# Kernel optimization log

Hardware: AMD Instinct MI355X
Metric: run time of the kernel (lower is better)

## Reference

```python
import jax, jax.numpy as jnp
import numpy as np

N, D, H, E, K = 65536, 128, 256, 32, 2


def setup_inputs() -> dict:
    key = jax.random.key(0)
    ks = jax.random.split(key, 7)
    s_in = 1.0 / np.sqrt(D)
    s_hid = 1.0 / np.sqrt(H)
    return {
        "x": jax.random.normal(ks[0], (N, D), dtype=jnp.float32),
        "W1": jax.random.uniform(ks[1], (E, D, H), jnp.float32, -s_in, s_in),
        "b1": jax.random.uniform(ks[2], (E, H), jnp.float32, -s_in, s_in),
        "W2": jax.random.uniform(ks[3], (E, H, D), jnp.float32, -s_hid, s_hid),
        "b2": jax.random.uniform(ks[4], (E, D), jnp.float32, -s_hid, s_hid),
        "Wr": jax.random.uniform(ks[5], (D, E), jnp.float32, -s_in, s_in),
        "br": jax.random.uniform(ks[6], (E,), jnp.float32, -s_in, s_in),
    }


def reference(x, W1, b1, W2, b2, Wr, br):
    # Router (eval mode: no gate noise)
    logits = x @ Wr + br                                  # [N, E]
    scores = jax.nn.softmax(logits, axis=-1)              # [N, E]
    topk_vals, topk_inds = jax.lax.top_k(scores, K)       # [N, K]

    # dispatch_mask: zeros scattered with top-k probs (scatter_ on dim 1)
    n = x.shape[0]
    dispatch_mask = jnp.zeros_like(scores).at[
        jnp.arange(n)[:, None], topk_inds
    ].set(topk_vals)                                      # [N, E]

    # Dense all-experts compute, as in the reference torch.stack
    h = jax.nn.relu(jnp.einsum("nd,edh->neh", x, W1) + b1)   # [N, E, H]
    expert_outputs = jnp.einsum("neh,ehd->ned", h, W2) + b2  # [N, E, D]

    output = jnp.einsum("ned,ne->nd", expert_outputs, dispatch_mask)  # [N, D]

    importance = dispatch_mask.sum(axis=0)                # [E]
    imp_mean = jnp.mean(importance)
    imp_var = jnp.var(importance, ddof=1)                 # torch.var is unbiased
    load_balancing_loss = imp_var / (imp_mean ** 2 + 1e-9)
    return output, load_balancing_loss
```

## Files before the change

### kernel.cpp

```cpp
#include <hip/hip_runtime.h>
#include <hip/hip_bf16.h>
#include <cstdint>
#include <cstddef>

#define N_TOK 65536
#define DIM 128
#define HID 256
#define NE 32
#define TOPK 2

typedef __bf16 bf16x8 __attribute__((ext_vector_type(8)));
typedef float f32x4 __attribute__((ext_vector_type(4)));
typedef unsigned uint4v __attribute__((ext_vector_type(4)));

__device__ __forceinline__ unsigned short f2bf(float f) {
  unsigned u = __builtin_bit_cast(unsigned, f);
  u += 0x7fffu + ((u >> 16) & 1u);
  return (unsigned short)(u >> 16);
}
__device__ __forceinline__ float bf2f(unsigned s) {
  return __builtin_bit_cast(float, s << 16);
}
__device__ __forceinline__ uint2 split2(float f0, float f1) {
  unsigned u0 = __builtin_bit_cast(unsigned, f0);
  unsigned u1 = __builtin_bit_cast(unsigned, f1);
  unsigned hi = (u0 >> 16) | (u1 & 0xffff0000u);
  float r0 = f0 - __builtin_bit_cast(float, u0 & 0xffff0000u);
  float r1 = f1 - __builtin_bit_cast(float, u1 & 0xffff0000u);
  unsigned lo = (__builtin_bit_cast(unsigned, r0) >> 16) |
                (__builtin_bit_cast(unsigned, r1) & 0xffff0000u);
  uint2 ret; ret.x = hi; ret.y = lo;
  return ret;
}

__global__ void k_zero_out(float* __restrict__ out) {
  int t = blockIdx.x * 256 + threadIdx.x;
  float4 z = make_float4(0.f, 0.f, 0.f, 0.f);
  float4* o4 = (float4*)out;
  o4[t] = z;
  o4[t + 1048576] = z;
}

__global__ void k_weights(const float* __restrict__ W1, const float* __restrict__ W2,
                          const float* __restrict__ Wr,
                          unsigned short* __restrict__ w1t, unsigned short* __restrict__ w2t,
                          double* __restrict__ wrt64, unsigned short* __restrict__ wrb,
                          float* __restrict__ ws32, int* __restrict__ n_suspect) {
  int b = blockIdx.x;
  if (b == 512) {
    if (threadIdx.x == 0) *n_suspect = 0;
#pragma unroll
    for (int j = 0; j < 16; ++j) {
      int idx = j * 256 + threadIdx.x;
      int e = idx >> 7, d = idx & 127;
      wrt64[idx] = (double)Wr[d * NE + e];
    }
#pragma unroll
    for (int j = 0; j < 16; ++j) {
      int idx = j * 256 + threadIdx.x;
      int k = idx >> 5, e = idx & 31;
      float w = Wr[k * NE + e];
      unsigned u = __builtin_bit_cast(unsigned, w);
      unsigned short hs = (unsigned short)(u >> 16);
      float r = w - __builtin_bit_cast(float, u & 0xffff0000u);
      unsigned short ls = (unsigned short)(__builtin_bit_cast(unsigned, r) >> 16);
      int nt = e >> 4, n = e & 15, kc = k >> 5, q = (k >> 3) & 3, jj = k & 7;
      size_t base = ((((size_t)nt * 4 + kc) * 4 + q) * 16 + n) * 8 + jj;
      wrb[base] = hs;
      wrb[8192 + base] = ls;
    }
    return;
  }
  if (b == 0 && threadIdx.x < 96) ws32[threadIdx.x] = 0.f;
  const float* in;
  unsigned short* out;
  int K, r0, c0;
  if (b < 256) {
    int e = b >> 3, tt = b & 7;
    in = W1 + (size_t)e * DIM * HID;
    out = w1t + (size_t)e * DIM * HID;
    K = HID;
    r0 = (tt >> 2) * 64; c0 = (tt & 3) * 64;
  } else {
    b -= 256;
    int e = b >> 3, tt = b & 7;
    in = W2 + (size_t)e * HID * DIM;
    out = w2t + (size_t)e * HID * DIM;
    K = DIM;
    r0 = (tt >> 1) * 64; c0 = (tt & 1) * 64;
  }
  __shared__ float tile[64][65];
  int t2 = threadIdx.x;
  int r = t2 >> 2, cs = (t2 & 3) * 16;
  const float* src = in + (size_t)(r0 + r) * K + c0 + cs;
#pragma unroll
  for (int j = 0; j < 4; ++j) {
    float4 v = *(const float4*)(src + j * 4);
    tile[r][cs + j * 4 + 0] = v.x;
    tile[r][cs + j * 4 + 1] = v.y;
    tile[r][cs + j * 4 + 2] = v.z;
    tile[r][cs + j * 4 + 3] = v.w;
  }
  __syncthreads();
#pragma unroll
  for (int p = 0; p < 2; ++p) {
    int orow = p * 32 + (t2 >> 3);
    int oc8 = (t2 & 7) * 8;
    int rr = r0 + oc8;
    unsigned pk[4];
#pragma unroll
    for (int q = 0; q < 4; ++q) {
      unsigned lo = f2bf(tile[oc8 + 2 * q][orow]);
      unsigned hi = f2bf(tile[oc8 + 2 * q + 1][orow]);
      pk[q] = lo | (hi << 16);
    }
    uint4 u;
    u.x = pk[0]; u.y = pk[1]; u.z = pk[2]; u.w = pk[3];
    size_t addr = (size_t)(rr >> 5) * (K * 32) + (size_t)(c0 + orow) * 32 + (rr & 31);
    *(uint4*)(out + addr) = u;
  }
}

__global__ __launch_bounds__(256) void k_router(
    const float* __restrict__ x, const unsigned short* __restrict__ wrb,
    const float* __restrict__ br, int* __restrict__ top_idx, float* __restrict__ top_val,
    int* __restrict__ suspects, int* __restrict__ n_suspect) {
  int t = threadIdx.x;
  int w = t >> 6, l = t & 63, quad = l >> 4, l15 = l & 15;
  int tok0 = blockIdx.x * 256 + w * 64;

  bf16x8 bfr[2][2][4];
#pragma unroll
  for (int s = 0; s < 2; ++s)
#pragma unroll
    for (int nt = 0; nt < 2; ++nt)
#pragma unroll
      for (int kc = 0; kc < 4; ++kc)
        bfr[s][nt][kc] = *(const bf16x8*)(wrb + s * 8192 +
                          ((((size_t)nt * 4 + kc) * 4 + quad) * 16 + l15) * 8);

  f32x4 acc[4][2];
#pragma unroll
  for (int a = 0; a < 4; ++a)
#pragma unroll
    for (int b = 0; b < 2; ++b) {
      f32x4 z = {0.f, 0.f, 0.f, 0.f};
      acc[a][b] = z;
    }

#pragma unroll
  for (int mt = 0; mt < 4; ++mt) {
    const float* xp = x + (size_t)(tok0 + mt * 16 + l15) * DIM + quad * 8;
    float4 va[4][2];
#pragma unroll
    for (int kc = 0; kc < 4; ++kc) {
      const float4* p = (const float4*)(xp + kc * 32);
      va[kc][0] = p[0];
      va[kc][1] = p[1];
    }
#pragma unroll
    for (int kc = 0; kc < 4; ++kc) {
      uint2 s0 = split2(va[kc][0].x, va[kc][0].y);
      uint2 s1 = split2(va[kc][0].z, va[kc][0].w);
      uint2 s2 = split2(va[kc][1].x, va[kc][1].y);
      uint2 s3 = split2(va[kc][1].z, va[kc][1].w);
      uint4v hu, lu;
      hu[0] = s0.x; lu[0] = s0.y;
      hu[1] = s1.x; lu[1] = s1.y;
      hu[2] = s2.x; lu[2] = s2.y;
      hu[3] = s3.x; lu[3] = s3.y;
      bf16x8 ahi = __builtin_bit_cast(bf16x8, hu);
      bf16x8 alo = __builtin_bit_cast(bf16x8, lu);
#pragma unroll
      for (int nt = 0; nt < 2; ++nt) {
        acc[mt][nt] = __builtin_amdgcn_mfma_f32_16x16x32_bf16(ahi, bfr[0][nt][kc], acc[mt][nt], 0, 0, 0);
        acc[mt][nt] = __builtin_amdgcn_mfma_f32_16x16x32_bf16(ahi, bfr[1][nt][kc], acc[mt][nt], 0, 0, 0);
        acc[mt][nt] = __builtin_amdgcn_mfma_f32_16x16x32_bf16(alo, bfr[0][nt][kc], acc[mt][nt], 0, 0, 0);
      }
    }
  }

  float brv0 = br[l15], brv1 = br[16 + l15];
  const float NINF = -3.0e38f;
#pragma unroll
  for (int mt = 0; mt < 4; ++mt) {
#pragma unroll
    for (int r = 0; r < 4; ++r) {
      float c0 = acc[mt][0][r] + brv0;
      float c1 = acc[mt][1][r] + brv1;
      float va = (c0 >= c1) ? c0 : c1;
      int ia = (c0 >= c1) ? l15 : 16 + l15;
#pragma unroll
      for (int off = 1; off < 16; off <<= 1) {
        float ov = __shfl_xor(va, off);
        int oi = __shfl_xor(ia, off);
        if (ov > va || (ov == va && oi < ia)) { va = ov; ia = oi; }
      }
      float v1 = va; int i1 = ia;
      float d0 = (i1 == l15) ? NINF : c0;
      float d1 = (i1 == 16 + l15) ? NINF : c1;
      float vb = (d0 >= d1) ? d0 : d1;
      int ib = (d0 >= d1) ? l15 : 16 + l15;
#pragma unroll
      for (int off = 1; off < 16; off <<= 1) {
        float ov = __shfl_xor(vb, off);
        int oi = __shfl_xor(ib, off);
        if (ov > vb || (ov == vb && oi < ib)) { vb = ov; ib = oi; }
      }
      float v2 = vb; int i2 = ib;
      float e0 = (i1 == l15 || i2 == l15) ? NINF : c0;
      float e1 = (i1 == 16 + l15 || i2 == 16 + l15) ? NINF : c1;
      float vc = (e0 >= e1) ? e0 : e1;
#pragma unroll
      for (int off = 1; off < 16; off <<= 1) {
        float ov = __shfl_xor(vc, off);
        vc = (ov > vc) ? ov : vc;
      }
      float s = __expf(c0 - v1) + __expf(c1 - v1);
#pragma unroll
      for (int off = 1; off < 16; off <<= 1) s += __shfl_xor(s, off);
      if (l15 == 0) {
        int n = tok0 + mt * 16 + quad * 4 + r;
        int2 ti; ti.x = i1; ti.y = i2;
        float2 tv; tv.x = 1.0f / s; tv.y = __expf(v2 - v1) / s;
        ((int2*)top_idx)[n] = ti;
        ((float2*)top_val)[n] = tv;
        if (v2 - vc < 2e-3f) {
          int sidx = atomicAdd(n_suspect, 1);
          suspects[sidx] = n;
        }
      }
    }
  }
}

__global__ __launch_bounds__(256) void k_router_fix(
    const float* __restrict__ x, const double* __restrict__ wrt64,
    const float* __restrict__ br, const int* __restrict__ suspects,
    const int* __restrict__ n_suspect, int* __restrict__ top_idx,
    float* __restrict__ top_val) {
  int t = threadIdx.x;
  int lt = t & 31;
  int gid = blockIdx.x * 8 + (t >> 5);
  int cnt = *n_suspect;
  const double* wcol = wrt64 + lt * DIM;
  for (int s = gid; s < cnt; s += 128 * 8) {
    int n = suspects[s];
    const float* xr = x + (size_t)n * DIM;
    double a = 0.0;
#pragma unroll 8
    for (int d = 0; d < DIM; ++d) a = fma((double)xr[d], wcol[d], a);
    double lv = a + (double)br[lt];

    double v1 = lv; int i1 = lt;
#pragma unroll
    for (int off = 16; off > 0; off >>= 1) {
      double ov = __shfl_xor(v1, off, 32);
      int oi = __shfl_xor(i1, off, 32);
      if (ov > v1 || (ov == v1 && oi < i1)) { v1 = ov; i1 = oi; }
    }
    double lv2 = (lt == i1) ? -1.0e300 : lv;
    double v2 = lv2; int i2 = lt;
#pragma unroll
    for (int off = 16; off > 0; off >>= 1) {
      double ov = __shfl_xor(v2, off, 32);
      int oi = __shfl_xor(i2, off, 32);
      if (ov > v2 || (ov == v2 && oi < i2)) { v2 = ov; i2 = oi; }
    }
    float p = expf((float)(lv - v1));
    float ssum = p;
#pragma unroll
    for (int off = 16; off > 0; off >>= 1) ssum += __shfl_xor(ssum, off, 32);
    if (lt == 0) {
      top_idx[n * 2 + 0] = i1;
      top_idx[n * 2 + 1] = i2;
      top_val[n * 2 + 0] = 1.0f / ssum;
      top_val[n * 2 + 1] = expf((float)(v2 - v1)) / ssum;
    }
  }
}

__global__ __launch_bounds__(256) void k_router_f64(const float* __restrict__ x,
                                                    const double* __restrict__ wrt64,
                                                    const float* __restrict__ br,
                                                    int* __restrict__ top_idx,
                                                    float* __restrict__ top_val) {
  int t = threadIdx.x;
  int lt = t & 31;
  int n = blockIdx.x * 8 + (t >> 5);
  const double* wcol = wrt64 + lt * DIM;
  const float* xr = x + (size_t)n * DIM;
  double a = 0.0;
#pragma unroll 8
  for (int d = 0; d < DIM; ++d) a = fma((double)xr[d], wcol[d], a);
  double lv = a + (double)br[lt];
  double v1 = lv; int i1 = lt;
#pragma unroll
  for (int off = 16; off > 0; off >>= 1) {
    double ov = __shfl_xor(v1, off, 32);
    int oi = __shfl_xor(i1, off, 32);
    if (ov > v1 || (ov == v1 && oi < i1)) { v1 = ov; i1 = oi; }
  }
  double lv2 = (lt == i1) ? -1.0e300 : lv;
  double v2 = lv2; int i2 = lt;
#pragma unroll
  for (int off = 16; off > 0; off >>= 1) {
    double ov = __shfl_xor(v2, off, 32);
    int oi = __shfl_xor(i2, off, 32);
    if (ov > v2 || (ov == v2 && oi < i2)) { v2 = ov; i2 = oi; }
  }
  float p = expf((float)(lv - v1));
  float ssum = p;
#pragma unroll
  for (int off = 16; off > 0; off >>= 1) ssum += __shfl_xor(ssum, off, 32);
  if (lt == 0) {
    top_idx[n * 2 + 0] = i1;
    top_idx[n * 2 + 1] = i2;
    top_val[n * 2 + 0] = 1.0f / ssum;
    top_val[n * 2 + 1] = expf((float)(v2 - v1)) / ssum;
  }
}

__global__ void k_hist(const int* __restrict__ top_idx, const float* __restrict__ top_val,
                       int* __restrict__ counts, float* __restrict__ importance) {
  __shared__ int hc[NE];
  __shared__ float hf[NE];
  int t = threadIdx.x;
  if (t < NE) { hc[t] = 0; hf[t] = 0.f; }
  __syncthreads();
#pragma unroll
  for (int j = 0; j < 2; ++j) {
    int i = (j * 256 + blockIdx.x) * 256 + t;
    int e = top_idx[i];
    atomicAdd(&hc[e], 1);
    atomicAdd(&hf[e], top_val[i]);
  }
  __syncthreads();
  if (t < NE) {
    atomicAdd(&counts[t], hc[t]);
    atomicAdd(&importance[t], hf[t]);
  }
}

__global__ void k_scan_loss(const int* __restrict__ counts, const float* __restrict__ importance,
                            int* __restrict__ offsets, float* __restrict__ out_loss) {
  int t = threadIdx.x;
  if (t < NE) {
    int pc = (counts[t] + 63) & ~63;
    int sc = pc;
#pragma unroll
    for (int off = 1; off < 32; off <<= 1) {
      int ov = __shfl_up(sc, off, 32);
      if (t >= off) sc += ov;
    }
    offsets[t] = sc - pc;
    if (t == NE - 1) offsets[NE] = sc;

    float imp = importance[t];
    float ssum = imp;
#pragma unroll
    for (int off = 16; off > 0; off >>= 1) ssum += __shfl_xor(ssum, off, 32);
    float mean = ssum / 32.0f;
    float dlt = imp - mean;
    float v = dlt * dlt;
#pragma unroll
    for (int off = 16; off > 0; off >>= 1) v += __shfl_xor(v, off, 32);
    float var = v / 31.0f;
    if (t == 0) *out_loss = var / (mean * mean + 1e-9f);
  }
}

__global__ void k_scatter(const int* __restrict__ top_idx, const float* __restrict__ top_val,
                          const int* __restrict__ offsets, int* __restrict__ cursors,
                          int* __restrict__ perm, float* __restrict__ gatev,
                          int* __restrict__ inv) {
  __shared__ int hist[NE], base[NE], cur[NE];
  int t = threadIdx.x;
  if (t < NE) { hist[t] = 0; cur[t] = 0; }
  __syncthreads();
#pragma unroll
  for (int j = 0; j < 4; ++j) {
    int i = blockIdx.x * 1024 + j * 256 + t;
    atomicAdd(&hist[top_idx[i]], 1);
  }
  __syncthreads();
  if (t < NE) base[t] = atomicAdd(&cursors[t], hist[t]);
  __syncthreads();
#pragma unroll
  for (int j = 0; j < 4; ++j) {
    int i = blockIdx.x * 1024 + j * 256 + t;
    int e = top_idx[i];
    int p = atomicAdd(&cur[e], 1);
    int pos = offsets[e] + base[e] + p;
    perm[pos] = i >> 1;
    gatev[pos] = top_val[i];
    inv[i] = pos;
  }
}

template <int YB>
__global__ __launch_bounds__(256, 2) void k_expert(
    const float* __restrict__ x, const unsigned short* __restrict__ w1t,
    const unsigned short* __restrict__ w2t, const float* __restrict__ b1,
    const float* __restrict__ b2, const int* __restrict__ offsets,
    const int* __restrict__ counts, const int* __restrict__ perm,
    const float* __restrict__ gatev, unsigned short* __restrict__ ybuf,
    float* __restrict__ out) {
  __shared__ __align__(16) unsigned char smem[49152];
  unsigned char* xa = smem;
  unsigned char* ha = smem + 16384;

  int slot0 = blockIdx.x * 64;
  if (slot0 >= offsets[NE]) return;
  int e = 0;
#pragma unroll
  for (int i = 1; i < NE; ++i)
    if (slot0 >= offsets[i]) e = i;
  int cnt = counts[e];
  int local0 = slot0 - offsets[e];
  int nvalid = min(64, cnt - local0);

  int t = threadIdx.x;
  int w = t >> 6;
  int l = t & 63;
  int quad = l >> 4;
  int l15 = l & 15;

  const unsigned short* w1e = w1t + (size_t)e * DIM * HID;
  bf16x8 w1f[4][4];
#pragma unroll
  for (int kc = 0; kc < 4; ++kc)
#pragma unroll
    for (int jt = 0; jt < 4; ++jt)
      w1f[kc][jt] = *(const bf16x8*)(w1e + kc * 8192 + (w * 64 + jt * 16 + l15) * 32 + quad * 8);

  {
    int r = t & 63;
    int half = t >> 6;
    unsigned pk[16];
    if (r < nvalid) {
      int token = perm[slot0 + r];
      const float* src = x + (size_t)token * DIM + half * 32;
#pragma unroll
      for (int q = 0; q < 8; ++q) {
        float4 v = ((const float4*)src)[q];
        pk[q * 2 + 0] = (unsigned)f2bf(v.x) | ((unsigned)f2bf(v.y) << 16);
        pk[q * 2 + 1] = (unsigned)f2bf(v.z) | ((unsigned)f2bf(v.w) << 16);
      }
    } else {
#pragma unroll
      for (int q = 0; q < 16; ++q) pk[q] = 0u;
    }
#pragma unroll
    for (int cc = 0; cc < 4; ++cc) {
      uint4 u;
      u.x = pk[cc * 4 + 0]; u.y = pk[cc * 4 + 1]; u.z = pk[cc * 4 + 2]; u.w = pk[cc * 4 + 3];
      *(uint4*)(xa + (half * 4 + cc) * 1024 + r * 16) = u;
    }
  }
  __syncthreads();

  f32x4 acc[4][4];
#pragma unroll
  for (int a = 0; a < 4; ++a)
#pragma unroll
    for (int b = 0; b < 4; ++b) {
      f32x4 z = {0.f, 0.f, 0.f, 0.f};
      acc[a][b] = z;
    }
#pragma unroll
  for (int kc = 0; kc < 4; ++kc) {
    bf16x8 af[4];
#pragma unroll
    for (int rt = 0; rt < 4; ++rt)
      af[rt] = *(const bf16x8*)(xa + (kc * 4 + quad) * 1024 + (rt * 16 + l15) * 16);
#pragma unroll
    for (int rt = 0; rt < 4; ++rt)
#pragma unroll
      for (int jt = 0; jt < 4; ++jt)
        acc[rt][jt] = __builtin_amdgcn_mfma_f32_16x16x32_bf16(af[rt], w1f[kc][jt], acc[rt][jt], 0, 0, 0);
  }

  const unsigned short* w2e = w2t + (size_t)e * HID * DIM;
  bf16x8 w2f[8][2];
#pragma unroll
  for (int hc = 0; hc < 8; ++hc)
#pragma unroll
    for (int jt = 0; jt < 2; ++jt)
      w2f[hc][jt] = *(const bf16x8*)(w2e + hc * 4096 + (w * 32 + jt * 16 + l15) * 32 + quad * 8);

  const float* b1e = b1 + e * HID;
#pragma unroll
  for (int jt = 0; jt < 4; ++jt) {
    int col = w * 64 + jt * 16 + l15;
    float b1v = b1e[col];
    int c = col >> 3;
    int byteoff = (col & 7) * 2;
#pragma unroll
    for (int rt = 0; rt < 4; ++rt) {
#pragma unroll
      for (int r = 0; r < 4; ++r) {
        int tokrow = rt * 16 + quad * 4 + r;
        float v = acc[rt][jt][r] + b1v;
        v = v > 0.f ? v : 0.f;
        *(unsigned short*)(ha + c * 1024 + tokrow * 16 + byteoff) = f2bf(v);
      }
    }
  }
  __syncthreads();

  f32x4 accc[4][2];
#pragma unroll
  for (int a = 0; a < 4; ++a)
#pragma unroll
    for (int b = 0; b < 2; ++b) {
      f32x4 z = {0.f, 0.f, 0.f, 0.f};
      accc[a][b] = z;
    }
#pragma unroll
  for (int hc = 0; hc < 8; ++hc) {
    bf16x8 ah[4];
#pragma unroll
    for (int rt = 0; rt < 4; ++rt)
      ah[rt] = *(const bf16x8*)(ha + (hc * 4 + quad) * 1024 + (rt * 16 + l15) * 16);
#pragma unroll
    for (int rt = 0; rt < 4; ++rt)
#pragma unroll
      for (int jt = 0; jt < 2; ++jt)
        accc[rt][jt] = __builtin_amdgcn_mfma_f32_16x16x32_bf16(ah[rt], w2f[hc][jt], accc[rt][jt], 0, 0, 0);
  }

  int dbase = w * 32;
  float b2v0 = b2[e * DIM + dbase + l15];
  float b2v1 = b2[e * DIM + dbase + 16 + l15];
#pragma unroll
  for (int rt = 0; rt < 4; ++rt) {
#pragma unroll
    for (int r = 0; r < 4; ++r) {
      int tokrow = rt * 16 + quad * 4 + r;
      if (tokrow < nvalid) {
        int pos = slot0 + tokrow;
        float g = gatev[pos];
        if (YB) {
          unsigned short* yrow = ybuf + (size_t)pos * DIM + dbase;
          yrow[l15] = f2bf(g * (accc[rt][0][r] + b2v0));
          yrow[16 + l15] = f2bf(g * (accc[rt][1][r] + b2v1));
        } else {
          int token = perm[pos];
          float* orow = out + (size_t)token * DIM + dbase;
          atomicAdd(&orow[l15], g * (accc[rt][0][r] + b2v0));
          atomicAdd(&orow[16 + l15], g * (accc[rt][1][r] + b2v1));
        }
      }
    }
  }
}

__global__ __launch_bounds__(256) void k_combine(const unsigned short* __restrict__ ybuf,
                                                 const int* __restrict__ inv,
                                                 float* __restrict__ out) {
  int t = threadIdx.x;
  int n = blockIdx.x * 16 + (t >> 4);
  int lane = t & 15;
  int p0 = inv[n * 2 + 0];
  int p1 = inv[n * 2 + 1];
  uint4 a = *((const uint4*)(ybuf + (size_t)p0 * DIM) + lane);
  uint4 b = *((const uint4*)(ybuf + (size_t)p1 * DIM) + lane);
  unsigned av[4] = {a.x, a.y, a.z, a.w}, bv[4] = {b.x, b.y, b.z, b.w};
  float r[8];
#pragma unroll
  for (int q = 0; q < 4; ++q) {
    r[q * 2 + 0] = bf2f(av[q] & 0xffffu) + bf2f(bv[q] & 0xffffu);
    r[q * 2 + 1] = bf2f(av[q] >> 16) + bf2f(bv[q] >> 16);
  }
  float* orow = out + (size_t)n * DIM + lane * 8;
  float4 w0 = {r[0], r[1], r[2], r[3]}, w1 = {r[4], r[5], r[6], r[7]};
  ((float4*)orow)[0] = w0;
  ((float4*)orow)[1] = w1;
}

extern "C" void kernel_launch(void* const* d_in, const int* in_sizes, int n_in,
                              void* d_out, int out_size, void* d_ws, size_t ws_size,
                              hipStream_t stream) {
  const float* x  = (const float*)d_in[0];
  const float* W1 = (const float*)d_in[1];
  const float* b1 = (const float*)d_in[2];
  const float* W2 = (const float*)d_in[3];
  const float* b2 = (const float*)d_in[4];
  const float* Wr = (const float*)d_in[5];
  const float* br = (const float*)d_in[6];
  float* out = (float*)d_out;

  char* ws = (char*)d_ws;
  float* importance   = (float*)(ws + 0);
  int*   counts       = (int*)(ws + 128);
  int*   cursors      = (int*)(ws + 256);
  int*   offsets      = (int*)(ws + 384);
  int*   top_idx      = (int*)(ws + 1024);
  float* top_val      = (float*)(ws + 525312);
  int*   perm         = (int*)(ws + 1049600);
  float* gatev        = (float*)(ws + 1582080);
  int*   inv          = (int*)(ws + 2114560);
  unsigned short* w1t = (unsigned short*)(ws + 2638848);
  unsigned short* w2t = (unsigned short*)(ws + 4736000);
  unsigned short* ybuf = (unsigned short*)(ws + 6833152);
  double* wrt64 = (double*)(ws + 6833152);
  unsigned short* wrb = (unsigned short*)(ws + 6833152 + 32768);
  int* suspects = (int*)(ws + 40911872);
  int* n_suspect = (int*)(ws + 41174016);
  const size_t NEEDED = 41174144;
  bool use_ybuf = ws_size >= NEEDED;

  hipLaunchKernelGGL(k_weights, dim3(513), dim3(256), 0, stream, W1, W2, Wr, w1t, w2t, wrt64,
                     wrb, (float*)ws, n_suspect);
  if (use_ybuf) {
    hipLaunchKernelGGL(k_router, dim3(256), dim3(256), 0, stream, x, wrb, br, top_idx, top_val,
                       suspects, n_suspect);
    hipLaunchKernelGGL(k_router_fix, dim3(128), dim3(256), 0, stream, x, wrt64, br, suspects,
                       n_suspect, top_idx, top_val);
  } else {
    hipLaunchKernelGGL(k_router_f64, dim3(8192), dim3(256), 0, stream, x, wrt64, br, top_idx,
                       top_val);
  }
  hipLaunchKernelGGL(k_hist, dim3(256), dim3(256), 0, stream, top_idx, top_val, counts, importance);
  hipLaunchKernelGGL(k_scan_loss, dim3(1), dim3(64), 0, stream, counts, importance, offsets,
                     out + (size_t)N_TOK * DIM);
  hipLaunchKernelGGL(k_scatter, dim3(128), dim3(256), 0, stream, top_idx, top_val, offsets,
                     cursors, perm, gatev, inv);
  if (use_ybuf) {
    hipLaunchKernelGGL((k_expert<1>), dim3(2080), dim3(256), 0, stream, x, w1t, w2t, b1, b2,
                       offsets, counts, perm, gatev, ybuf, out);
    hipLaunchKernelGGL(k_combine, dim3(4096), dim3(256), 0, stream, ybuf, inv, out);
  } else {
    hipLaunchKernelGGL(k_zero_out, dim3(4096), dim3(256), 0, stream, out);
    hipLaunchKernelGGL((k_expert<0>), dim3(2080), dim3(256), 0, stream, x, w1t, w2t, b1, b2,
                       offsets, counts, perm, gatev, ybuf, out);
  }
}
```

Before: 216.4 us.

## Fuse histogram into router, merge scan into scatter, persistent per-expert blocks

Expert counts and importance are now accumulated inside the router (with corrections in the fix kernel), and the offset scan plus loss are folded into the scatter kernel. This removes the hist and scan launches and the offsets/inv buffers. The expert kernel becomes persistent: 16 blocks per expert loop over 64-token chunks, loading weights and biases once and prefetching the next chunk's x rows. ybuf is indexed by token*2+k so combine reads rows contiguously. The trade-offs are possible load imbalance when experts have uneven token counts and extra atomics in the router.

```diff
diff --git a/kernel.cpp b/kernel.cpp
--- a/kernel.cpp
+++ b/kernel.cpp
@@ -124,8 +124,13 @@
 __global__ __launch_bounds__(256) void k_router(
     const float* __restrict__ x, const unsigned short* __restrict__ wrb,
     const float* __restrict__ br, int* __restrict__ top_idx, float* __restrict__ top_val,
-    int* __restrict__ suspects, int* __restrict__ n_suspect) {
+    int* __restrict__ suspects, int* __restrict__ n_suspect,
+    int* __restrict__ counts, float* __restrict__ importance) {
+  __shared__ int hc[NE];
+  __shared__ float hf[NE];
   int t = threadIdx.x;
+  if (t < NE) { hc[t] = 0; hf[t] = 0.f; }
+  __syncthreads();
   int w = t >> 6, l = t & 63, quad = l >> 4, l15 = l & 15;
   int tok0 = blockIdx.x * 256 + w * 64;
 
@@ -221,10 +226,16 @@
       for (int off = 1; off < 16; off <<= 1) s += __shfl_xor(s, off);
       if (l15 == 0) {
         int n = tok0 + mt * 16 + quad * 4 + r;
+        float g1 = 1.0f / s;
+        float g2 = __expf(v2 - v1) / s;
         int2 ti; ti.x = i1; ti.y = i2;
-        float2 tv; tv.x = 1.0f / s; tv.y = __expf(v2 - v1) / s;
+        float2 tv; tv.x = g1; tv.y = g2;
         ((int2*)top_idx)[n] = ti;
         ((float2*)top_val)[n] = tv;
+        atomicAdd(&hc[i1], 1);
+        atomicAdd(&hc[i2], 1);
+        atomicAdd(&hf[i1], g1);
+        atomicAdd(&hf[i2], g2);
         if (v2 - vc < 2e-3f) {
           int sidx = atomicAdd(n_suspect, 1);
           suspects[sidx] = n;
@@ -232,13 +243,19 @@
       }
     }
   }
+  __syncthreads();
+  if (t < NE) {
+    atomicAdd(&counts[t], hc[t]);
+    atomicAdd(&importance[t], hf[t]);
+  }
 }
 
 __global__ __launch_bounds__(256) void k_router_fix(
     const float* __restrict__ x, const double* __restrict__ wrt64,
     const float* __restrict__ br, const int* __restrict__ suspects,
     const int* __restrict__ n_suspect, int* __restrict__ top_idx,
-    float* __restrict__ top_val) {
+    float* __restrict__ top_val, int* __restrict__ counts,
+    float* __restrict__ importance) {
   int t = threadIdx.x;
   int lt = t & 31;
   int gid = blockIdx.x * 8 + (t >> 5);
@@ -272,10 +289,18 @@
 #pragma unroll
     for (int off = 16; off > 0; off >>= 1) ssum += __shfl_xor(ssum, off, 32);
     if (lt == 0) {
+      int i1o = top_idx[n * 2 + 0], i2o = top_idx[n * 2 + 1];
+      float g1o = top_val[n * 2 + 0], g2o = top_val[n * 2 + 1];
+      float g1 = 1.0f / ssum;
+      float g2 = expf((float)(v2 - v1)) / ssum;
       top_idx[n * 2 + 0] = i1;
       top_idx[n * 2 + 1] = i2;
-      top_val[n * 2 + 0] = 1.0f / ssum;
-      top_val[n * 2 + 1] = expf((float)(v2 - v1)) / ssum;
+      top_val[n * 2 + 0] = g1;
+      top_val[n * 2 + 1] = g2;
+      atomicAdd(&counts[i1o], -1); atomicAdd(&counts[i2o], -1);
+      atomicAdd(&counts[i1], 1);   atomicAdd(&counts[i2], 1);
+      atomicAdd(&importance[i1o], -g1o); atomicAdd(&importance[i2o], -g2o);
+      atomicAdd(&importance[i1], g1);    atomicAdd(&importance[i2], g2);
     }
   }
 }
@@ -342,8 +367,68 @@
   }
 }
 
-__global__ void k_scan_loss(const int* __restrict__ counts, const float* __restrict__ importance,
-                            int* __restrict__ offsets, float* __restrict__ out_loss) {
+__global__ void k_scatter(const int* __restrict__ top_idx, const float* __restrict__ top_val,
+                          const int* __restrict__ counts, const float* __restrict__ importance,
+                          int* __restrict__ cursors, int* __restrict__ perm,
+                          float* __restrict__ gatev, float* __restrict__ out_loss) {
+  __shared__ int hist[NE], base[NE], cur[NE], off_s[NE];
+  int t = threadIdx.x;
+  if (t < NE) {
+    hist[t] = 0; cur[t] = 0;
+    int pc = (counts[t] + 63) & ~63;
+    int sc = pc;
+#pragma unroll
+    for (int off = 1; off < 32; off <<= 1) {
+      int ov = __shfl_up(sc, off, 32);
+      if (t >= off) sc += ov;
+    }
+    off_s[t] = sc - pc;
+    if (blockIdx.x == 0) {
+      float imp = importance[t];
+      float ssum = imp;
+#pragma unroll
+      for (int off = 16; off > 0; off >>= 1) ssum += __shfl_xor(ssum, off, 32);
+      float mean = ssum / 32.0f;
+      float dlt = imp - mean;
+      float v = dlt * dlt;
+#pragma unroll
+      for (int off = 16; off > 0; off >>= 1) v += __shfl_xor(v, off, 32);
+      float var = v / 31.0f;
+      if (t == 0) *out_loss = var / (mean * mean + 1e-9f);
+    }
+  }
+  __syncthreads();
+#pragma unroll
+  for (int j = 0; j < 4; ++j) {
+    int i = blockIdx.x * 1024 + j * 256 + t;
+    atomicAdd(&hist[top_idx[i]], 1);
+  }
+  __syncthreads();
+  if (t < NE) base[t] = atomicAdd(&cursors[t], hist[t]);
+  __syncthreads();
+#pragma unroll
+  for (int j = 0; j < 4; ++j) {
+    int i = blockIdx.x * 1024 + j * 256 + t;
+    int e = top_idx[i];
+    int p = atomicAdd(&cur[e], 1);
+    int pos = off_s[e] + base[e] + p;
+    perm[pos] = i;
+    gatev[pos] = top_val[i];
+  }
+}
+
+template <int YB>
+__global__ __launch_bounds__(256, 2) void k_expert(
+    const float* __restrict__ x, const unsigned short* __restrict__ w1t,
+    const unsigned short* __restrict__ w2t, const float* __restrict__ b1,
+    const float* __restrict__ b2, const int* __restrict__ counts,
+    const int* __restrict__ perm, const float* __restrict__ gatev,
+    unsigned short* __restrict__ ybuf, float* __restrict__ out) {
+  __shared__ __align__(16) unsigned char smem[49152];
+  unsigned char* xa = smem;
+  unsigned char* ha = smem + 16384;
+  __shared__ int off_s[NE];
+
   int t = threadIdx.x;
   if (t < NE) {
     int pc = (counts[t] + 63) & ~63;
@@ -353,78 +438,18 @@
       int ov = __shfl_up(sc, off, 32);
       if (t >= off) sc += ov;
     }
-    offsets[t] = sc - pc;
-    if (t == NE - 1) offsets[NE] = sc;
-
-    float imp = importance[t];
-    float ssum = imp;
-#pragma unroll
-    for (int off = 16; off > 0; off >>= 1) ssum += __shfl_xor(ssum, off, 32);
-    float mean = ssum / 32.0f;
-    float dlt = imp - mean;
-    float v = dlt * dlt;
-#pragma unroll
-    for (int off = 16; off > 0; off >>= 1) v += __shfl_xor(v, off, 32);
-    float var = v / 31.0f;
-    if (t == 0) *out_loss = var / (mean * mean + 1e-9f);
-  }
-}
-
-__global__ void k_scatter(const int* __restrict__ top_idx, const float* __restrict__ top_val,
-                          const int* __restrict__ offsets, int* __restrict__ cursors,
-                          int* __restrict__ perm, float* __restrict__ gatev,
-                          int* __restrict__ inv) {
-  __shared__ int hist[NE], base[NE], cur[NE];
-  int t = threadIdx.x;
-  if (t < NE) { hist[t] = 0; cur[t] = 0; }
-  __syncthreads();
-#pragma unroll
-  for (int j = 0; j < 4; ++j) {
-    int i = blockIdx.x * 1024 + j * 256 + t;
-    atomicAdd(&hist[top_idx[i]], 1);
-  }
-  __syncthreads();
-  if (t < NE) base[t] = atomicAdd(&cursors[t], hist[t]);
-  __syncthreads();
-#pragma unroll
-  for (int j = 0; j < 4; ++j) {
-    int i = blockIdx.x * 1024 + j * 256 + t;
-    int e = top_idx[i];
-    int p = atomicAdd(&cur[e], 1);
-    int pos = offsets[e] + base[e] + p;
-    perm[pos] = i >> 1;
-    gatev[pos] = top_val[i];
-    inv[i] = pos;
-  }
-}
-
-template <int YB>
-__global__ __launch_bounds__(256, 2) void k_expert(
-    const float* __restrict__ x, const unsigned short* __restrict__ w1t,
-    const unsigned short* __restrict__ w2t, const float* __restrict__ b1,
-    const float* __restrict__ b2, const int* __restrict__ offsets,
-    const int* __restrict__ counts, const int* __restrict__ perm,
-    const float* __restrict__ gatev, unsigned short* __restrict__ ybuf,
-    float* __restrict__ out) {
-  __shared__ __align__(16) unsigned char smem[49152];
-  unsigned char* xa = smem;
-  unsigned char* ha = smem + 16384;
-
-  int slot0 = blockIdx.x * 64;
-  if (slot0 >= offsets[NE]) return;
-  int e = 0;
-#pragma unroll
-  for (int i = 1; i < NE; ++i)
-    if (slot0 >= offsets[i]) e = i;
+    off_s[t] = sc - pc;
+  }
+  __syncthreads();
+
+  int e = blockIdx.x >> 4;
+  int sub = blockIdx.x & 15;
   int cnt = counts[e];
-  int local0 = slot0 - offsets[e];
-  int nvalid = min(64, cnt - local0);
-
-  int t = threadIdx.x;
-  int w = t >> 6;
-  int l = t & 63;
-  int quad = l >> 4;
-  int l15 = l & 15;
+  int slotbase = off_s[e];
+  int nch = (cnt + 63) >> 6;
+
+  int w = t >> 6, l = t & 63, quad = l >> 4, l15 = l & 15;
+  int r = t & 63, half = t >> 6;
 
   const unsigned short* w1e = w1t + (size_t)e * DIM * HID;
   bf16x8 w1f[4][4];
@@ -433,14 +458,29 @@
 #pragma unroll
     for (int jt = 0; jt < 4; ++jt)
       w1f[kc][jt] = *(const bf16x8*)(w1e + kc * 8192 + (w * 64 + jt * 16 + l15) * 32 + quad * 8);
-
+  const unsigned short* w2e = w2t + (size_t)e * HID * DIM;
+  bf16x8 w2f[8][2];
+#pragma unroll
+  for (int hc = 0; hc < 8; ++hc)
+#pragma unroll
+    for (int jt = 0; jt < 2; ++jt)
+      w2f[hc][jt] = *(const bf16x8*)(w2e + hc * 4096 + (w * 32 + jt * 16 + l15) * 32 + quad * 8);
+
+  const float* b1e = b1 + e * HID;
+  float b1v[4];
+#pragma unroll
+  for (int jt = 0; jt < 4; ++jt) b1v[jt] = b1e[w * 64 + jt * 16 + l15];
+  int dbase = w * 32;
+  float b2v0 = b2[e * DIM + dbase + l15];
+  float b2v1 = b2[e * DIM + dbase + 16 + l15];
+
+  int c = sub;
+  unsigned pk[16];
   {
-    int r = t & 63;
-    int half = t >> 6;
-    unsigned pk[16];
-    if (r < nvalid) {
-      int token = perm[slot0 + r];
-      const float* src = x + (size_t)token * DIM + half * 32;
+    bool hv = (c < nch) && (r < cnt - c * 64);
+    if (hv) {
+      int pmv = perm[slotbase + c * 64 + r];
+      const float* src = x + (size_t)(pmv >> 1) * DIM + half * 32;
 #pragma unroll
       for (int q = 0; q < 8; ++q) {
         float4 v = ((const float4*)src)[q];
@@ -451,121 +491,133 @@
 #pragma unroll
       for (int q = 0; q < 16; ++q) pk[q] = 0u;
     }
+  }
+
+  while (c < nch) {
 #pragma unroll
     for (int cc = 0; cc < 4; ++cc) {
       uint4 u;
       u.x = pk[cc * 4 + 0]; u.y = pk[cc * 4 + 1]; u.z = pk[cc * 4 + 2]; u.w = pk[cc * 4 + 3];
       *(uint4*)(xa + (half * 4 + cc) * 1024 + r * 16) = u;
     }
-  }
-  __syncthreads();
-
-  f32x4 acc[4][4];
-#pragma unroll
-  for (int a = 0; a < 4; ++a)
-#pragma unroll
-    for (int b = 0; b < 4; ++b) {
-      f32x4 z = {0.f, 0.f, 0.f, 0.f};
-      acc[a][b] = z;
-    }
-#pragma unroll
-  for (int kc = 0; kc < 4; ++kc) {
-    bf16x8 af[4];
-#pragma unroll
-    for (int rt = 0; rt < 4; ++rt)
-      af[rt] = *(const bf16x8*)(xa + (kc * 4 + quad) * 1024 + (rt * 16 + l15) * 16);
-#pragma unroll
-    for (int rt = 0; rt < 4; ++rt)
-#pragma unroll
-      for (int jt = 0; jt < 4; ++jt)
-        acc[rt][jt] = __builtin_amdgcn_mfma_f32_16x16x32_bf16(af[rt], w1f[kc][jt], acc[rt][jt], 0, 0, 0);
-  }
-
-  const unsigned short* w2e = w2t + (size_t)e * HID * DIM;
-  bf16x8 w2f[8][2];
-#pragma unroll
-  for (int hc = 0; hc < 8; ++hc)
-#pragma unroll
-    for (int jt = 0; jt < 2; ++jt)
-      w2f[hc][jt] = *(const bf16x8*)(w2e + hc * 4096 + (w * 32 + jt * 16 + l15) * 32 + quad * 8);
-
-  const float* b1e = b1 + e * HID;
-#pragma unroll
-  for (int jt = 0; jt < 4; ++jt) {
-    int col = w * 64 + jt * 16 + l15;
-    float b1v = b1e[col];
-    int c = col >> 3;
-    int byteoff = (col & 7) * 2;
+    __syncthreads();
+
+    int cn = c + 16;
+    bool hvn = (cn < nch) && (r < cnt - cn * 64);
+    float4 nx[8];
+    if (hvn) {
+      int pmn = perm[slotbase + cn * 64 + r];
+      const float* srcn = x + (size_t)(pmn >> 1) * DIM + half * 32;
+#pragma unroll
+      for (int q = 0; q < 8; ++q) nx[q] = ((const float4*)srcn)[q];
+    }
+
+    f32x4 acc[4][4];
+#pragma unroll
+    for (int a = 0; a < 4; ++a)
+#pragma unroll
+      for (int b = 0; b < 4; ++b) {
+        f32x4 z = {0.f, 0.f, 0.f, 0.f};
+        acc[a][b] = z;
+      }
+#pragma unroll
+    for (int kc = 0; kc < 4; ++kc) {
+      bf16x8 af[4];
+#pragma unroll
+      for (int rt = 0; rt < 4; ++rt)
+        af[rt] = *(const bf16x8*)(xa + (kc * 4 + quad) * 1024 + (rt * 16 + l15) * 16);
+#pragma unroll
+      for (int rt = 0; rt < 4; ++rt)
+#pragma unroll
+        for (int jt = 0; jt < 4; ++jt)
+          acc[rt][jt] = __builtin_amdgcn_mfma_f32_16x16x32_bf16(af[rt], w1f[kc][jt], acc[rt][jt], 0, 0, 0);
+    }
+
+#pragma unroll
+    for (int jt = 0; jt < 4; ++jt) {
+      int col = w * 64 + jt * 16 + l15;
+      int cidx = col >> 3;
+      int byteoff = (col & 7) * 2;
+#pragma unroll
+      for (int rt = 0; rt < 4; ++rt) {
+#pragma unroll
+        for (int rr = 0; rr < 4; ++rr) {
+          int tokrow = rt * 16 + quad * 4 + rr;
+          float v = acc[rt][jt][rr] + b1v[jt];
+          v = v > 0.f ? v : 0.f;
+          *(unsigned short*)(ha + cidx * 1024 + tokrow * 16 + byteoff) = f2bf(v);
+        }
+      }
+    }
+    __syncthreads();
+
+    f32x4 accc[4][2];
+#pragma unroll
+    for (int a = 0; a < 4; ++a)
+#pragma unroll
+      for (int b = 0; b < 2; ++b) {
+        f32x4 z = {0.f, 0.f, 0.f, 0.f};
+        accc[a][b] = z;
+      }
+#pragma unroll
+    for (int hc = 0; hc < 8; ++hc) {
+      bf16x8 ah[4];
+#pragma unroll
+      for (int rt = 0; rt < 4; ++rt)
+        ah[rt] = *(const bf16x8*)(ha + (hc * 4 + quad) * 1024 + (rt * 16 + l15) * 16);
+#pragma unroll
+      for (int rt = 0; rt < 4; ++rt)
+#pragma unroll
+        for (int jt = 0; jt < 2; ++jt)
+          accc[rt][jt] = __builtin_amdgcn_mfma_f32_16x16x32_bf16(ah[rt], w2f[hc][jt], accc[rt][jt], 0, 0, 0);
+    }
+
+    int slot0 = slotbase + c * 64;
+    int nv = cnt - c * 64; nv = nv > 64 ? 64 : nv;
 #pragma unroll
     for (int rt = 0; rt < 4; ++rt) {
 #pragma unroll
-      for (int r = 0; r < 4; ++r) {
-        int tokrow = rt * 16 + quad * 4 + r;
-        float v = acc[rt][jt][r] + b1v;
-        v = v > 0.f ? v : 0.f;
-        *(unsigned short*)(ha + c * 1024 + tokrow * 16 + byteoff) = f2bf(v);
-      }
-    }
-  }
-  __syncthreads();
-
-  f32x4 accc[4][2];
-#pragma unroll
-  for (int a = 0; a < 4; ++a)
-#pragma unroll
-    for (int b = 0; b < 2; ++b) {
-      f32x4 z = {0.f, 0.f, 0.f, 0.f};
-      accc[a][b] = z;
-    }
-#pragma unroll
-  for (int hc = 0; hc < 8; ++hc) {
-    bf16x8 ah[4];
-#pragma unroll
-    for (int rt = 0; rt < 4; ++rt)
-      ah[rt] = *(const bf16x8*)(ha + (hc * 4 + quad) * 1024 + (rt * 16 + l15) * 16);
-#pragma unroll
-    for (int rt = 0; rt < 4; ++rt)
-#pragma unroll
-      for (int jt = 0; jt < 2; ++jt)
-        accc[rt][jt] = __builtin_amdgcn_mfma_f32_16x16x32_bf16(ah[rt], w2f[hc][jt], accc[rt][jt], 0, 0, 0);
-  }
-
-  int dbase = w * 32;
-  float b2v0 = b2[e * DIM + dbase + l15];
-  float b2v1 = b2[e * DIM + dbase + 16 + l15];
-#pragma unroll
-  for (int rt = 0; rt < 4; ++rt) {
-#pragma unroll
-    for (int r = 0; r < 4; ++r) {
-      int tokrow = rt * 16 + quad * 4 + r;
-      if (tokrow < nvalid) {
-        int pos = slot0 + tokrow;
-        float g = gatev[pos];
-        if (YB) {
-          unsigned short* yrow = ybuf + (size_t)pos * DIM + dbase;
-          yrow[l15] = f2bf(g * (accc[rt][0][r] + b2v0));
-          yrow[16 + l15] = f2bf(g * (accc[rt][1][r] + b2v1));
-        } else {
-          int token = perm[pos];
-          float* orow = out + (size_t)token * DIM + dbase;
-          atomicAdd(&orow[l15], g * (accc[rt][0][r] + b2v0));
-          atomicAdd(&orow[16 + l15], g * (accc[rt][1][r] + b2v1));
+      for (int rr = 0; rr < 4; ++rr) {
+        int tokrow = rt * 16 + quad * 4 + rr;
+        if (tokrow < nv) {
+          int pos = slot0 + tokrow;
+          int pmv = perm[pos];
+          float g = gatev[pos];
+          if (YB) {
+            unsigned short* yrow = ybuf + (size_t)pmv * DIM + dbase;
+            yrow[l15] = f2bf(g * (accc[rt][0][rr] + b2v0));
+            yrow[16 + l15] = f2bf(g * (accc[rt][1][rr] + b2v1));
+          } else {
+            float* orow = out + (size_t)(pmv >> 1) * DIM + dbase;
+            atomicAdd(&orow[l15], g * (accc[rt][0][rr] + b2v0));
+            atomicAdd(&orow[16 + l15], g * (accc[rt][1][rr] + b2v1));
+          }
         }
       }
     }
+
+    if (hvn) {
+#pragma unroll
+      for (int q = 0; q < 8; ++q) {
+        pk[q * 2 + 0] = (unsigned)f2bf(nx[q].x) | ((unsigned)f2bf(nx[q].y) << 16);
+        pk[q * 2 + 1] = (unsigned)f2bf(nx[q].z) | ((unsigned)f2bf(nx[q].w) << 16);
+      }
+    } else {
+#pragma unroll
+      for (int q = 0; q < 16; ++q) pk[q] = 0u;
+    }
+    c = cn;
   }
 }
 
 __global__ __launch_bounds__(256) void k_combine(const unsigned short* __restrict__ ybuf,
-                                                 const int* __restrict__ inv,
                                                  float* __restrict__ out) {
   int t = threadIdx.x;
   int n = blockIdx.x * 16 + (t >> 4);
   int lane = t & 15;
-  int p0 = inv[n * 2 + 0];
-  int p1 = inv[n * 2 + 1];
-  uint4 a = *((const uint4*)(ybuf + (size_t)p0 * DIM) + lane);
-  uint4 b = *((const uint4*)(ybuf + (size_t)p1 * DIM) + lane);
+  const uint4* rows = (const uint4*)(ybuf + (size_t)(2 * n) * DIM);
+  uint4 a = rows[lane];
+  uint4 b = rows[16 + lane];
   unsigned av[4] = {a.x, a.y, a.z, a.w}, bv[4] = {b.x, b.y, b.z, b.w};
   float r[8];
 #pragma unroll
@@ -595,45 +647,42 @@
   float* importance   = (float*)(ws + 0);
   int*   counts       = (int*)(ws + 128);
   int*   cursors      = (int*)(ws + 256);
-  int*   offsets      = (int*)(ws + 384);
   int*   top_idx      = (int*)(ws + 1024);
   float* top_val      = (float*)(ws + 525312);
   int*   perm         = (int*)(ws + 1049600);
   float* gatev        = (float*)(ws + 1582080);
-  int*   inv          = (int*)(ws + 2114560);
-  unsigned short* w1t = (unsigned short*)(ws + 2638848);
-  unsigned short* w2t = (unsigned short*)(ws + 4736000);
-  unsigned short* ybuf = (unsigned short*)(ws + 6833152);
-  double* wrt64 = (double*)(ws + 6833152);
-  unsigned short* wrb = (unsigned short*)(ws + 6833152 + 32768);
-  int* suspects = (int*)(ws + 40911872);
-  int* n_suspect = (int*)(ws + 41174016);
-  const size_t NEEDED = 41174144;
+  unsigned short* w1t = (unsigned short*)(ws + 2114560);
+  unsigned short* w2t = (unsigned short*)(ws + 4211712);
+  unsigned short* ybuf = (unsigned short*)(ws + 6308864);
+  double* wrt64 = (double*)(ws + 6308864);
+  unsigned short* wrb = (unsigned short*)(ws + 6308864 + 32768);
+  int* suspects = (int*)(ws + 39863296);
+  int* n_suspect = (int*)(ws + 40125440);
+  const size_t NEEDED = 40125568;
   bool use_ybuf = ws_size >= NEEDED;
 
   hipLaunchKernelGGL(k_weights, dim3(513), dim3(256), 0, stream, W1, W2, Wr, w1t, w2t, wrt64,
                      wrb, (float*)ws, n_suspect);
   if (use_ybuf) {
     hipLaunchKernelGGL(k_router, dim3(256), dim3(256), 0, stream, x, wrb, br, top_idx, top_val,
-                       suspects, n_suspect);
+                       suspects, n_suspect, counts, importance);
     hipLaunchKernelGGL(k_router_fix, dim3(128), dim3(256), 0, stream, x, wrt64, br, suspects,
-                       n_suspect, top_idx, top_val);
+                       n_suspect, top_idx, top_val, counts, importance);
   } else {
     hipLaunchKernelGGL(k_router_f64, dim3(8192), dim3(256), 0, stream, x, wrt64, br, top_idx,
                        top_val);
-  }
-  hipLaunchKernelGGL(k_hist, dim3(256), dim3(256), 0, stream, top_idx, top_val, counts, importance);
-  hipLaunchKernelGGL(k_scan_loss, dim3(1), dim3(64), 0, stream, counts, importance, offsets,
-                     out + (size_t)N_TOK * DIM);
-  hipLaunchKernelGGL(k_scatter, dim3(128), dim3(256), 0, stream, top_idx, top_val, offsets,
-                     cursors, perm, gatev, inv);
+    hipLaunchKernelGGL(k_hist, dim3(256), dim3(256), 0, stream, top_idx, top_val, counts,
+                       importance);
+  }
+  hipLaunchKernelGGL(k_scatter, dim3(128), dim3(256), 0, stream, top_idx, top_val, counts,
+                     importance, cursors, perm, gatev, out + (size_t)N_TOK * DIM);
   if (use_ybuf) {
-    hipLaunchKernelGGL((k_expert<1>), dim3(2080), dim3(256), 0, stream, x, w1t, w2t, b1, b2,
-                       offsets, counts, perm, gatev, ybuf, out);
-    hipLaunchKernelGGL(k_combine, dim3(4096), dim3(256), 0, stream, ybuf, inv, out);
+    hipLaunchKernelGGL((k_expert<1>), dim3(512), dim3(256), 0, stream, x, w1t, w2t, b1, b2,
+                       counts, perm, gatev, ybuf, out);
+    hipLaunchKernelGGL(k_combine, dim3(4096), dim3(256), 0, stream, ybuf, out);
   } else {
     hipLaunchKernelGGL(k_zero_out, dim3(4096), dim3(256), 0, stream, out);
-    hipLaunchKernelGGL((k_expert<0>), dim3(2080), dim3(256), 0, stream, x, w1t, w2t, b1, b2,
-                       offsets, counts, perm, gatev, ybuf, out);
-  }
-}
+    hipLaunchKernelGGL((k_expert<0>), dim3(512), dim3(256), 0, stream, x, w1t, w2t, b1, b2,
+                       counts, perm, gatev, ybuf, out);
+  }
+}
```

Result: slower. 298.4 us (+37.9%).
